# Performance work log

Hardware: AMD Instinct MI355X
Metric: run time of the kernel (lower is better)

## Reference

```python
import jax, jax.numpy as jnp
import numpy as np
import math

D_MODEL = 1024
NUM_HEADS = 16
D_K = D_MODEL // NUM_HEADS
MAX_SEQ_LEN = 2048
ROPE_THETA = 10000.0
BATCH = 4
SEQ = 2048


def _rope_buffers():
    inv_freq = 1.0 / (ROPE_THETA ** (jnp.arange(0, D_K, 2, dtype=jnp.float32) / D_K))
    positions = jnp.arange(MAX_SEQ_LEN, dtype=jnp.float32)
    angles = jnp.einsum('i,j->ij', positions, inv_freq)  # [max_seq_len, d_k/2]
    return jnp.cos(angles), jnp.sin(angles)


def setup_inputs() -> dict:
    key = jax.random.key(0)
    kx, kq, kk, kv, ko = jax.random.split(key, 5)
    std = math.sqrt(2.0 / (D_MODEL + D_MODEL))
    x = jax.random.normal(kx, (BATCH, SEQ, D_MODEL), dtype=jnp.float32)
    pos_ids = jnp.broadcast_to(jnp.arange(SEQ, dtype=jnp.int64), (BATCH, SEQ))
    Wq = jax.random.normal(kq, (D_MODEL, D_MODEL), dtype=jnp.float32) * std
    Wk = jax.random.normal(kk, (D_MODEL, D_MODEL), dtype=jnp.float32) * std
    Wv = jax.random.normal(kv, (D_MODEL, D_MODEL), dtype=jnp.float32) * std
    Wo = jax.random.normal(ko, (D_MODEL, D_MODEL), dtype=jnp.float32) * std
    cos, sin = _rope_buffers()
    return {"x": x, "pos_ids": pos_ids, "Wq": Wq, "Wk": Wk, "Wv": Wv, "Wo": Wo, "cos": cos, "sin": sin}


def _apply_rope(t, pos_ids, cos, sin):
    # t: [B, H, S, D_K]; interleaved (even, odd) pair rotation, as in the torch module
    cp = cos[pos_ids][:, None, :, :]  # [B,1,S,D_K/2]
    sp = sin[pos_ids][:, None, :, :]
    tr = t.reshape(*t.shape[:-1], D_K // 2, 2)
    t0, t1 = tr[..., 0], tr[..., 1]
    rot = jnp.stack((t0 * cp - t1 * sp, t0 * sp + t1 * cp), axis=-1)
    return rot.reshape(t.shape)


def reference(x, pos_ids, Wq, Wk, Wv, Wo, cos, sin):
    B, S, _ = x.shape
    def proj(W):
        return jnp.matmul(x, W.T).reshape(B, S, NUM_HEADS, D_K).transpose(0, 2, 1, 3)
    Q = _apply_rope(proj(Wq), pos_ids, cos, sin)
    K = _apply_rope(proj(Wk), pos_ids, cos, sin)
    V = proj(Wv)
    scores = jnp.einsum('bhqd,bhkd->bhqk', Q, K) / math.sqrt(D_K)
    causal = jnp.tril(jnp.ones((S, S), dtype=bool))
    scores = jnp.where(causal, scores, -jnp.inf)
    attn = jax.nn.softmax(scores, axis=-1)
    out = jnp.einsum('bhqk,bhkd->bhqd', attn, V)
    out = out.transpose(0, 2, 1, 3).reshape(B, S, D_MODEL)
    return jnp.matmul(out, Wo.T)
```

## Files before the change

### kernel.cpp

```cpp
#include <hip/hip_runtime.h>
#include <hip/hip_bf16.h>

typedef __bf16 bf16;
typedef __bf16 bf16x4 __attribute__((ext_vector_type(4)));
typedef __bf16 bf16x8 __attribute__((ext_vector_type(8)));
typedef float f32x4 __attribute__((ext_vector_type(4)));
typedef unsigned int u32;

#define BATCH 4
#define SEQN 2048
#define NH 16
#define DK 64
#define DM 1024
#define MROWS (BATCH*SEQN)

__device__ __forceinline__ void async16(bf16* lds, const bf16* g) {
  __builtin_amdgcn_global_load_lds(
      (const __attribute__((address_space(1))) u32*)g,
      (__attribute__((address_space(3))) u32*)lds, 16, 0, 0);
}

__global__ void cvt_all_kernel(const float4* __restrict__ x,  const float4* __restrict__ wq,
                               const float4* __restrict__ wk, const float4* __restrict__ wv,
                               const float4* __restrict__ wo,
                               bf16x4* __restrict__ xb, bf16x4* __restrict__ wqkvb,
                               bf16x4* __restrict__ wob) {
  const int NX = MROWS*DM/4, NW = DM*DM/4;
  int i = blockIdx.x*256 + threadIdx.x;
  const float4* s; bf16x4* d; int j;
  if (i < NX)             { s = x;  d = xb;         j = i; }
  else if (i < NX+NW)     { s = wq; d = wqkvb;      j = i-NX; }
  else if (i < NX+2*NW)   { s = wk; d = wqkvb+NW;   j = i-NX-NW; }
  else if (i < NX+3*NW)   { s = wv; d = wqkvb+2*NW; j = i-NX-2*NW; }
  else if (i < NX+4*NW)   { s = wo; d = wob;        j = i-NX-3*NW; }
  else return;
  float4 f = s[j];
  bf16x4 v;
  v[0] = (bf16)f.x; v[1] = (bf16)f.y; v[2] = (bf16)f.z; v[3] = (bf16)f.w;
  d[j] = v;
}

#define BM 128
#define BN 128

__device__ __forceinline__ void gemm_core(const bf16* __restrict__ A, const bf16* __restrict__ Bt,
                                          int Kdim, int r0, int c0,
                                          bf16* As, bf16* Bs, f32x4 acc[4][4]) {
  const int tid  = threadIdx.x;
  const int wave = tid >> 6, lane = tid & 63;
  const int quad = lane >> 4, lc = lane & 15;
  const int wm = (wave >> 1)*64, wn = (wave & 1)*64;
  for (int k0 = 0; k0 < Kdim; k0 += 64) {
#pragma unroll
    for (int i = 0; i < 4; ++i) {
      int L = i*256 + tid;
      int row = L >> 3;
      int dc  = (L & 7) ^ (row & 7);
      bf16* lbase = As + (size_t)(i*256 + wave*64)*8;
      async16(lbase, A  + (size_t)(r0+row)*Kdim + k0 + dc*8);
      bf16* lbase2 = Bs + (size_t)(i*256 + wave*64)*8;
      async16(lbase2, Bt + (size_t)(c0+row)*Kdim + k0 + dc*8);
    }
    __syncthreads();
#pragma unroll
    for (int kk = 0; kk < 2; ++kk) {
      const int dc = kk*4 + quad;
      bf16x8 af[4], bfr[4];
#pragma unroll
      for (int mt = 0; mt < 4; ++mt) {
        int mr = wm + mt*16 + lc;
        af[mt] = *(const bf16x8*)(As + (size_t)(mr*8 + (dc ^ (mr & 7)))*8);
      }
#pragma unroll
      for (int nt = 0; nt < 4; ++nt) {
        int nr = wn + nt*16 + lc;
        bfr[nt] = *(const bf16x8*)(Bs + (size_t)(nr*8 + (dc ^ (nr & 7)))*8);
      }
#pragma unroll
      for (int mt = 0; mt < 4; ++mt)
#pragma unroll
        for (int nt = 0; nt < 4; ++nt)
          acc[mt][nt] = __builtin_amdgcn_mfma_f32_16x16x32_bf16(af[mt], bfr[nt], acc[mt][nt], 0, 0, 0);
    }
    __syncthreads();
  }
}

#define VS 136
__global__ __launch_bounds__(256) void gemm_qkv_kernel(const bf16* __restrict__ A,
    const bf16* __restrict__ Bt, const float* __restrict__ cosb, const float* __restrict__ sinb,
    bf16* __restrict__ Q, bf16* __restrict__ K, bf16* __restrict__ Vt) {
  __shared__ __align__(16) bf16 smem[128*VS];
  bf16* As = smem;
  bf16* Bs = smem + BM*64;
  f32x4 acc[4][4] = {};
  const int r0 = blockIdx.y*BM, c0 = blockIdx.x*BN;
  gemm_core(A, Bt, DM, r0, c0, As, Bs, acc);
  const int tid  = threadIdx.x;
  const int wave = tid >> 6, lane = tid & 63;
  const int quad = lane >> 4, lc = lane & 15;
  const int wm = (wave >> 1)*64, wn = (wave & 1)*64;
  const int which = c0 >> 10;
  if (which < 2) {
    bf16* T = which == 0 ? Q : K;
#pragma unroll
    for (int mt = 0; mt < 4; ++mt)
#pragma unroll
      for (int r = 0; r < 4; ++r) {
        int gr = r0 + wm + mt*16 + quad*4 + r;
        int b = gr >> 11, s = gr & (SEQN-1);
#pragma unroll
        for (int nt = 0; nt < 4; ++nt) {
          int gc = c0 + wn + nt*16 + lc;
          int c = gc & (DM-1), h = c >> 6, d = c & 63, p = d >> 1;
          float cc = cosb[s*32 + p], ss = sinb[s*32 + p];
          float v  = acc[mt][nt][r];
          float ov = __shfl_xor(v, 1, 64);
          float outv = ((lc & 1) == 0) ? (v*cc - ov*ss) : (ov*ss + v*cc);
          T[(((size_t)(b*NH + h))*SEQN + s)*DK + d] = (bf16)outv;
        }
      }
  } else {
#pragma unroll
    for (int mt = 0; mt < 4; ++mt)
#pragma unroll
      for (int nt = 0; nt < 4; ++nt) {
        int col = wn + nt*16 + lc;
        bf16x4 vv;
#pragma unroll
        for (int r = 0; r < 4; ++r) vv[r] = (bf16)acc[mt][nt][r];
        *(bf16x4*)(smem + (size_t)col*VS + wm + mt*16 + quad*4) = vv;
      }
    __syncthreads();
    const int b = r0 >> 11, s_base = r0 & (SEQN-1);
    const int h0 = (c0 & (DM-1)) >> 6;
#pragma unroll
    for (int it = 0; it < 8; ++it) {
      int dall = it*16 + (tid >> 4);
      int s_off = (tid & 15)*8;
      bf16x8 vv = *(const bf16x8*)(smem + (size_t)dall*VS + s_off);
      int h = h0 + (dall >> 6), d = dall & 63;
      *(bf16x8*)(Vt + (((size_t)(b*NH + h))*DK + d)*SEQN + s_base + s_off) = vv;
    }
  }
}

__global__ __launch_bounds__(256) void gemm_out_kernel(const bf16* __restrict__ A,
    const bf16* __restrict__ Bt, float* __restrict__ C) {
  __shared__ __align__(16) bf16 As[BM*64];
  __shared__ __align__(16) bf16 Bs[BN*64];
  f32x4 acc[4][4] = {};
  const int r0 = blockIdx.y*BM, c0 = blockIdx.x*BN;
  gemm_core(A, Bt, DM, r0, c0, As, Bs, acc);
  const int tid  = threadIdx.x;
  const int wave = tid >> 6, lane = tid & 63;
  const int quad = lane >> 4, lc = lane & 15;
  const int wm = (wave >> 1)*64, wn = (wave & 1)*64;
#pragma unroll
  for (int mt = 0; mt < 4; ++mt)
#pragma unroll
    for (int nt = 0; nt < 4; ++nt)
#pragma unroll
      for (int r = 0; r < 4; ++r) {
        int gr = r0 + wm + mt*16 + quad*4 + r;
        int gc = c0 + wn + nt*16 + lc;
        C[(size_t)gr*DM + gc] = acc[mt][nt][r];
      }
}

__global__ __launch_bounds__(256, 3) void attn_kernel(const bf16* __restrict__ Q,
    const bf16* __restrict__ K, const bf16* __restrict__ Vt, bf16* __restrict__ Oa) {
  __shared__ __align__(16) bf16 Ks[2][64*64];
  __shared__ __align__(16) bf16 Vs[2][64*64];
  __shared__ __align__(16) bf16 Pw[4][32*72];
  const int tid  = threadIdx.x;
  const int w = tid >> 6, lane = tid & 63;
  const int quad = lane >> 4, lc = lane & 15;
  const int bh = blockIdx.x;
  const int qt = (SEQN/128 - 1) - blockIdx.y;
  const int q0 = qt*128;
  const int qr0 = q0 + w*32;
  const bf16* Qp = Q  + (size_t)bh*SEQN*DK;
  const bf16* Kp = K  + (size_t)bh*SEQN*DK;
  const bf16* Vp = Vt + (size_t)bh*DK*SEQN;
  const float SC = 0.125f * 1.44269504f;
  bf16x8 aq[2][2];
#pragma unroll
  for (int mt = 0; mt < 2; ++mt)
#pragma unroll
    for (int kk = 0; kk < 2; ++kk) {
      bf16x8 raw = *(const bf16x8*)(Qp + (size_t)(qr0 + mt*16 + lc)*DK + kk*32 + quad*8);
#pragma unroll
      for (int j = 0; j < 8; ++j) raw[j] = (bf16)((float)raw[j] * SC);
      aq[mt][kk] = raw;
    }
  f32x4 o[2][4] = {};
  float lrow[2][4] = {};
  bf16* P = Pw[w];
  const int nsteps = 2*(qt + 1);

  auto stage = [&](int kt, int buf) {
#pragma unroll
    for (int j = 0; j < 2; ++j) {
      int L = j*256 + w*64 + lane;
      int row = L >> 3;
      int s8  = (L & 7) ^ (row & 7);
      bf16* kb = &Ks[buf][(size_t)(j*256 + w*64)*8];
      async16(kb, Kp + (size_t)(kt*64 + row)*DK + s8*8);
      bf16* vb = &Vs[buf][(size_t)(j*256 + w*64)*8];
      async16(vb, Vp + (size_t)row*SEQN + kt*64 + s8*8);
    }
  };

  stage(0, 0);
  for (int kt = 0; kt < nsteps; ++kt) {
    const int k0 = kt*64;
    const int cbuf = kt & 1;
    __syncthreads();
    if (kt + 1 < nsteps) stage(kt + 1, cbuf ^ 1);
    if (k0 <= qr0 + 31) {
      const bf16* Kt = Ks[cbuf];
      const bf16* Vc = Vs[cbuf];
      const int lastkey = qr0 + 31;
      f32x4 st[2][4] = {};
#pragma unroll
      for (int kk = 0; kk < 2; ++kk) {
        const int dc = kk*4 + quad;
        bf16x8 bk[4];
#pragma unroll
        for (int nt = 0; nt < 4; ++nt) {
          if (k0 + nt*16 <= lastkey) {
            int kr = nt*16 + lc;
            bk[nt] = *(const bf16x8*)(Kt + (size_t)(kr*8 + (dc ^ (kr & 7)))*8);
          }
        }
#pragma unroll
        for (int nt = 0; nt < 4; ++nt) {
          if (k0 + nt*16 <= lastkey) {
#pragma unroll
            for (int mt = 0; mt < 2; ++mt)
              st[mt][nt] = __builtin_amdgcn_mfma_f32_16x16x32_bf16(aq[mt][kk], bk[nt], st[mt][nt], 0, 0, 0);
          }
        }
      }
#pragma unroll
      for (int mt = 0; mt < 2; ++mt) {
        const int rmin = qr0 + mt*16, rmax = rmin + 15;
#pragma unroll
        for (int nt = 0; nt < 4; ++nt) {
          const int kmin = k0 + nt*16, kmax = kmin + 15;
          f32x4 p;
          if (kmax <= rmin) {
#pragma unroll
            for (int r = 0; r < 4; ++r) p[r] = exp2f(st[mt][nt][r]);
          } else if (kmin > rmax) {
            p = f32x4{0.f, 0.f, 0.f, 0.f};
          } else {
            const int key = kmin + lc;
#pragma unroll
            for (int r = 0; r < 4; ++r) {
              float v = exp2f(st[mt][nt][r]);
              p[r] = (key > rmin + quad*4 + r) ? 0.f : v;
            }
          }
          st[mt][nt] = p;
#pragma unroll
          for (int r = 0; r < 4; ++r) lrow[mt][r] += p[r];
        }
      }
#pragma unroll
      for (int mt = 0; mt < 2; ++mt)
#pragma unroll
        for (int r = 0; r < 4; ++r)
#pragma unroll
          for (int nt = 0; nt < 4; ++nt)
            P[(mt*16 + quad*4 + r)*72 + nt*16 + lc] = (bf16)st[mt][nt][r];
      asm volatile("s_waitcnt lgkmcnt(0)" ::: "memory");
#pragma unroll
      for (int kk = 0; kk < 2; ++kk) {
        if (k0 + kk*32 <= lastkey) {
          bf16x8 ap[2];
#pragma unroll
          for (int mt = 0; mt < 2; ++mt)
            ap[mt] = *(const bf16x8*)(P + (mt*16 + lc)*72 + kk*32 + quad*8);
          const int kc = kk*4 + quad;
          bf16x8 bv[4];
#pragma unroll
          for (int nb = 0; nb < 4; ++nb) {
            int dr = nb*16 + lc;
            bv[nb] = *(const bf16x8*)(Vc + (size_t)(dr*8 + (kc ^ (dr & 7)))*8);
          }
#pragma unroll
          for (int mt = 0; mt < 2; ++mt)
#pragma unroll
            for (int nb = 0; nb < 4; ++nb)
              o[mt][nb] = __builtin_amdgcn_mfma_f32_16x16x32_bf16(ap[mt], bv[nb], o[mt][nb], 0, 0, 0);
        }
      }
      asm volatile("s_waitcnt lgkmcnt(0)" ::: "memory");
    }
  }
#pragma unroll
  for (int off = 1; off < 16; off <<= 1)
#pragma unroll
    for (int mt = 0; mt < 2; ++mt)
#pragma unroll
      for (int r = 0; r < 4; ++r)
        lrow[mt][r] += __shfl_xor(lrow[mt][r], off, 64);
  const int b = bh >> 4, h = bh & 15;
#pragma unroll
  for (int mt = 0; mt < 2; ++mt)
#pragma unroll
    for (int r = 0; r < 4; ++r) {
      float inv = 1.f / lrow[mt][r];
      int qrow = qr0 + mt*16 + quad*4 + r;
      size_t rowoff = ((size_t)b*SEQN + qrow)*DM + h*DK;
#pragma unroll
      for (int nb = 0; nb < 4; ++nb)
        Oa[rowoff + nb*16 + lc] = (bf16)(o[mt][nb][r]*inv);
    }
}

extern "C" void kernel_launch(void* const* d_in, const int* in_sizes, int n_in,
                              void* d_out, int out_size, void* d_ws, size_t ws_size,
                              hipStream_t stream) {
  const float* x    = (const float*)d_in[0];
  const float* Wq   = (const float*)d_in[2];
  const float* Wk   = (const float*)d_in[3];
  const float* Wv   = (const float*)d_in[4];
  const float* Wo   = (const float*)d_in[5];
  const float* cosb = (const float*)d_in[6];
  const float* sinb = (const float*)d_in[7];
  float* out = (float*)d_out;

  char* ws = (char*)d_ws;
  const size_t SZ_X  = (size_t)MROWS*DM*2;
  const size_t SZ_W  = (size_t)DM*DM*2;
  bf16* xb   = (bf16*)(ws);
  bf16* wqkv = (bf16*)(ws + SZ_X);
  bf16* wo_b = (bf16*)(ws + SZ_X + 3*SZ_W);
  bf16* Qb   = (bf16*)(ws + SZ_X + 4*SZ_W);
  bf16* Kb   = (bf16*)(ws + 2*SZ_X + 4*SZ_W);
  bf16* Vtb  = (bf16*)(ws + 3*SZ_X + 4*SZ_W);
  bf16* Oa   = (bf16*)(ws + 4*SZ_X + 4*SZ_W);

  {
    const int NX = MROWS*DM/4, NW = DM*DM/4;
    int nblk = (NX + 4*NW + 255)/256;
    cvt_all_kernel<<<nblk, 256, 0, stream>>>((const float4*)x, (const float4*)Wq,
        (const float4*)Wk, (const float4*)Wv, (const float4*)Wo,
        (bf16x4*)xb, (bf16x4*)wqkv, (bf16x4*)wo_b);
  }
  gemm_qkv_kernel<<<dim3(3*DM/BN, MROWS/BM), 256, 0, stream>>>(xb, wqkv, cosb, sinb, Qb, Kb, Vtb);
  attn_kernel<<<dim3(BATCH*NH, SEQN/128), 256, 0, stream>>>(Qb, Kb, Vtb, Oa);
  gemm_out_kernel<<<dim3(DM/BN, MROWS/BM), 256, 0, stream>>>(Oa, wo_b, out);
}
```

Before: 267.7 us.

## Rewrite projection GEMMs as 256x256 tiles with double-buffered async LDS pipeline

Replaces the 128x128 single-buffered GEMM core used by the QKV and output projections with a 256x256 tile over 512 threads. The new core double-buffers A/B in LDS, issues async global-to-LDS loads one or two k-steps ahead with explicit vmcnt waits, and raises wave priority around the MFMA blocks. The aim is to overlap memory traffic with matrix math and improve operand reuse. The cost is more LDS (128KB per block) and more registers, which leaves far fewer blocks in flight: the output GEMM launches only 128 blocks and the QKV GEMM 384. The V-transpose epilogue is split into two passes to fit.

```diff
diff --git a/kernel.cpp b/kernel.cpp
--- a/kernel.cpp
+++ b/kernel.cpp
@@ -40,71 +40,112 @@
   d[j] = v;
 }
 
-#define BM 128
-#define BN 128
-
-__device__ __forceinline__ void gemm_core(const bf16* __restrict__ A, const bf16* __restrict__ Bt,
-                                          int Kdim, int r0, int c0,
-                                          bf16* As, bf16* Bs, f32x4 acc[4][4]) {
+__device__ __forceinline__ void stage_half(bf16* slot, const bf16* src) {
+  const int tid = threadIdx.x; const int w = tid >> 6;
+#pragma unroll
+  for (int j = 0; j < 2; ++j) {
+    int L = j*512 + tid;
+    int row = L >> 3;
+    int dc  = (L & 7) ^ (row & 7);
+    async16(slot + (size_t)(j*512 + w*64)*8, src + (size_t)row*DM + dc*8);
+  }
+}
+
+__device__ __forceinline__ void gemm_core256(const bf16* __restrict__ Ag,
+    const bf16* __restrict__ Bg, int r0, int c0, bf16* sm, f32x4 (&acc)[8][4]) {
   const int tid  = threadIdx.x;
-  const int wave = tid >> 6, lane = tid & 63;
-  const int quad = lane >> 4, lc = lane & 15;
-  const int wm = (wave >> 1)*64, wn = (wave & 1)*64;
-  for (int k0 = 0; k0 < Kdim; k0 += 64) {
-#pragma unroll
-    for (int i = 0; i < 4; ++i) {
-      int L = i*256 + tid;
-      int row = L >> 3;
-      int dc  = (L & 7) ^ (row & 7);
-      bf16* lbase = As + (size_t)(i*256 + wave*64)*8;
-      async16(lbase, A  + (size_t)(r0+row)*Kdim + k0 + dc*8);
-      bf16* lbase2 = Bs + (size_t)(i*256 + wave*64)*8;
-      async16(lbase2, Bt + (size_t)(c0+row)*Kdim + k0 + dc*8);
-    }
-    __syncthreads();
-#pragma unroll
-    for (int kk = 0; kk < 2; ++kk) {
-      const int dc = kk*4 + quad;
-      bf16x8 af[4], bfr[4];
-#pragma unroll
-      for (int mt = 0; mt < 4; ++mt) {
-        int mr = wm + mt*16 + lc;
-        af[mt] = *(const bf16x8*)(As + (size_t)(mr*8 + (dc ^ (mr & 7)))*8);
-      }
-#pragma unroll
-      for (int nt = 0; nt < 4; ++nt) {
-        int nr = wn + nt*16 + lc;
-        bfr[nt] = *(const bf16x8*)(Bs + (size_t)(nr*8 + (dc ^ (nr & 7)))*8);
-      }
-#pragma unroll
-      for (int mt = 0; mt < 4; ++mt)
-#pragma unroll
-        for (int nt = 0; nt < 4; ++nt)
-          acc[mt][nt] = __builtin_amdgcn_mfma_f32_16x16x32_bf16(af[mt], bfr[nt], acc[mt][nt], 0, 0, 0);
-    }
-    __syncthreads();
+  const int lane = tid & 63, quad = lane >> 4, lc = lane & 15;
+  const int w = tid >> 6;
+  const int wm = (w >> 2)*128, wn = (w & 3)*64;
+  const int NT = DM/64;
+  bf16* As[2] = { sm,         sm + 16384 };
+  bf16* Bs[2] = { sm + 32768, sm + 49152 };
+
+  auto stA = [&](int t, int h) {
+    int tt = t < NT ? t : NT-1;
+    stage_half(As[t&1] + h*8192, Ag + (size_t)(r0 + h*128)*DM + tt*64);
+  };
+  auto stB = [&](int t, int h) {
+    int tt = t < NT ? t : NT-1;
+    stage_half(Bs[t&1] + h*8192, Bg + (size_t)(c0 + h*128)*DM + tt*64);
+  };
+
+  stA(0,0); stA(0,1); stB(0,0); stB(0,1);
+  stA(1,0); stA(1,1); stB(1,0);
+  asm volatile("s_waitcnt vmcnt(6)" ::: "memory");
+  __builtin_amdgcn_sched_barrier(0);
+  __builtin_amdgcn_s_barrier();
+  __builtin_amdgcn_sched_barrier(0);
+
+  for (int t = 0; t < NT; ++t) {
+    const bf16* Ab = As[t&1];
+    const bf16* Bb = Bs[t&1];
+    stB(t+1, 1);
+    bf16x8 af[8], bb[4];
+#pragma unroll
+    for (int mt = 0; mt < 8; ++mt) {
+      int row = wm + mt*16 + lc;
+      af[mt] = *(const bf16x8*)(Ab + (size_t)((row<<3) + (quad ^ (row & 7)))*8);
+    }
+#pragma unroll
+    for (int nt = 0; nt < 4; ++nt) {
+      int row = wn + nt*16 + lc;
+      bb[nt] = *(const bf16x8*)(Bb + (size_t)((row<<3) + (quad ^ (row & 7)))*8);
+    }
+    __builtin_amdgcn_s_setprio(1);
+#pragma unroll
+    for (int mt = 0; mt < 8; ++mt)
+#pragma unroll
+      for (int nt = 0; nt < 4; ++nt)
+        acc[mt][nt] = __builtin_amdgcn_mfma_f32_16x16x32_bf16(af[mt], bb[nt], acc[mt][nt], 0, 0, 0);
+    __builtin_amdgcn_s_setprio(0);
+    bf16x8 af2[8], bb2[4];
+#pragma unroll
+    for (int mt = 0; mt < 8; ++mt) {
+      int row = wm + mt*16 + lc;
+      af2[mt] = *(const bf16x8*)(Ab + (size_t)((row<<3) + ((4 + quad) ^ (row & 7)))*8);
+    }
+#pragma unroll
+    for (int nt = 0; nt < 4; ++nt) {
+      int row = wn + nt*16 + lc;
+      bb2[nt] = *(const bf16x8*)(Bb + (size_t)((row<<3) + ((4 + quad) ^ (row & 7)))*8);
+    }
+    asm volatile("s_waitcnt lgkmcnt(0)" ::: "memory");
+    __builtin_amdgcn_sched_barrier(0);
+    __builtin_amdgcn_s_barrier();
+    __builtin_amdgcn_sched_barrier(0);
+    stA(t+2, 0); stA(t+2, 1); stB(t+2, 0);
+    __builtin_amdgcn_s_setprio(1);
+#pragma unroll
+    for (int mt = 0; mt < 8; ++mt)
+#pragma unroll
+      for (int nt = 0; nt < 4; ++nt)
+        acc[mt][nt] = __builtin_amdgcn_mfma_f32_16x16x32_bf16(af2[mt], bb2[nt], acc[mt][nt], 0, 0, 0);
+    __builtin_amdgcn_s_setprio(0);
+    asm volatile("s_waitcnt vmcnt(6)" ::: "memory");
+    __builtin_amdgcn_sched_barrier(0);
+    __builtin_amdgcn_s_barrier();
+    __builtin_amdgcn_sched_barrier(0);
   }
 }
 
 #define VS 136
-__global__ __launch_bounds__(256) void gemm_qkv_kernel(const bf16* __restrict__ A,
+__global__ __launch_bounds__(512, 2) void gemm_qkv_kernel(const bf16* __restrict__ A,
     const bf16* __restrict__ Bt, const float* __restrict__ cosb, const float* __restrict__ sinb,
     bf16* __restrict__ Q, bf16* __restrict__ K, bf16* __restrict__ Vt) {
-  __shared__ __align__(16) bf16 smem[128*VS];
-  bf16* As = smem;
-  bf16* Bs = smem + BM*64;
-  f32x4 acc[4][4] = {};
-  const int r0 = blockIdx.y*BM, c0 = blockIdx.x*BN;
-  gemm_core(A, Bt, DM, r0, c0, As, Bs, acc);
+  __shared__ __align__(16) bf16 sm[65536];
+  f32x4 acc[8][4] = {};
+  const int r0 = blockIdx.y*256, c0 = blockIdx.x*256;
+  gemm_core256(A, Bt, r0, c0, sm, acc);
   const int tid  = threadIdx.x;
-  const int wave = tid >> 6, lane = tid & 63;
-  const int quad = lane >> 4, lc = lane & 15;
-  const int wm = (wave >> 1)*64, wn = (wave & 1)*64;
+  const int lane = tid & 63, quad = lane >> 4, lc = lane & 15;
+  const int w = tid >> 6;
+  const int wm = (w >> 2)*128, wn = (w & 3)*64;
   const int which = c0 >> 10;
   if (which < 2) {
     bf16* T = which == 0 ? Q : K;
 #pragma unroll
-    for (int mt = 0; mt < 4; ++mt)
+    for (int mt = 0; mt < 8; ++mt)
 #pragma unroll
       for (int r = 0; r < 4; ++r) {
         int gr = r0 + wm + mt*16 + quad*4 + r;
@@ -121,43 +162,51 @@
         }
       }
   } else {
-#pragma unroll
-    for (int mt = 0; mt < 4; ++mt)
-#pragma unroll
-      for (int nt = 0; nt < 4; ++nt) {
-        int col = wn + nt*16 + lc;
-        bf16x4 vv;
-#pragma unroll
-        for (int r = 0; r < 4; ++r) vv[r] = (bf16)acc[mt][nt][r];
-        *(bf16x4*)(smem + (size_t)col*VS + wm + mt*16 + quad*4) = vv;
-      }
+    asm volatile("s_waitcnt vmcnt(0)" ::: "memory");
+    __builtin_amdgcn_sched_barrier(0);
     __syncthreads();
     const int b = r0 >> 11, s_base = r0 & (SEQN-1);
     const int h0 = (c0 & (DM-1)) >> 6;
 #pragma unroll
-    for (int it = 0; it < 8; ++it) {
-      int dall = it*16 + (tid >> 4);
-      int s_off = (tid & 15)*8;
-      bf16x8 vv = *(const bf16x8*)(smem + (size_t)dall*VS + s_off);
-      int h = h0 + (dall >> 6), d = dall & 63;
-      *(bf16x8*)(Vt + (((size_t)(b*NH + h))*DK + d)*SEQN + s_base + s_off) = vv;
+    for (int p = 0; p < 2; ++p) {
+      if ((w >> 2) == p) {
+#pragma unroll
+        for (int mt = 0; mt < 8; ++mt)
+#pragma unroll
+          for (int nt = 0; nt < 4; ++nt) {
+            int col = wn + nt*16 + lc;
+            bf16x4 vv;
+#pragma unroll
+            for (int r = 0; r < 4; ++r) vv[r] = (bf16)acc[mt][nt][r];
+            *(bf16x4*)(sm + (size_t)col*VS + mt*16 + quad*4) = vv;
+          }
+      }
+      __syncthreads();
+#pragma unroll
+      for (int it = 0; it < 8; ++it) {
+        int dall = it*32 + (tid >> 4);
+        int s_off = (tid & 15)*8;
+        bf16x8 vv = *(const bf16x8*)(sm + (size_t)dall*VS + s_off);
+        int h = h0 + (dall >> 6), d = dall & 63;
+        *(bf16x8*)(Vt + (((size_t)(b*NH + h))*DK + d)*SEQN + s_base + p*128 + s_off) = vv;
+      }
+      __syncthreads();
     }
   }
 }
 
-__global__ __launch_bounds__(256) void gemm_out_kernel(const bf16* __restrict__ A,
+__global__ __launch_bounds__(512, 2) void gemm_out_kernel(const bf16* __restrict__ A,
     const bf16* __restrict__ Bt, float* __restrict__ C) {
-  __shared__ __align__(16) bf16 As[BM*64];
-  __shared__ __align__(16) bf16 Bs[BN*64];
-  f32x4 acc[4][4] = {};
-  const int r0 = blockIdx.y*BM, c0 = blockIdx.x*BN;
-  gemm_core(A, Bt, DM, r0, c0, As, Bs, acc);
+  __shared__ __align__(16) bf16 sm[65536];
+  f32x4 acc[8][4] = {};
+  const int r0 = blockIdx.y*256, c0 = blockIdx.x*256;
+  gemm_core256(A, Bt, r0, c0, sm, acc);
   const int tid  = threadIdx.x;
-  const int wave = tid >> 6, lane = tid & 63;
-  const int quad = lane >> 4, lc = lane & 15;
-  const int wm = (wave >> 1)*64, wn = (wave & 1)*64;
-#pragma unroll
-  for (int mt = 0; mt < 4; ++mt)
+  const int lane = tid & 63, quad = lane >> 4, lc = lane & 15;
+  const int w = tid >> 6;
+  const int wm = (w >> 2)*128, wn = (w & 3)*64;
+#pragma unroll
+  for (int mt = 0; mt < 8; ++mt)
 #pragma unroll
     for (int nt = 0; nt < 4; ++nt)
 #pragma unroll
@@ -351,7 +400,7 @@
         (const float4*)Wk, (const float4*)Wv, (const float4*)Wo,
         (bf16x4*)xb, (bf16x4*)wqkv, (bf16x4*)wo_b);
   }
-  gemm_qkv_kernel<<<dim3(3*DM/BN, MROWS/BM), 256, 0, stream>>>(xb, wqkv, cosb, sinb, Qb, Kb, Vtb);
+  gemm_qkv_kernel<<<dim3(3*DM/256, MROWS/256), 512, 0, stream>>>(xb, wqkv, cosb, sinb, Qb, Kb, Vtb);
   attn_kernel<<<dim3(BATCH*NH, SEQN/128), 256, 0, stream>>>(Qb, Kb, Vtb, Oa);
-  gemm_out_kernel<<<dim3(DM/BN, MROWS/BM), 256, 0, stream>>>(Oa, wo_b, out);
-}
+  gemm_out_kernel<<<dim3(DM/256, MROWS/256), 512, 0, stream>>>(Oa, wo_b, out);
+}
```

Measured after the change: 329.8 us. 1.23x slower.
